# Performance work log

Hardware: AMD Instinct MI355X
Metric: run time of the kernel (lower is better)

## Reference

```python
import math
import jax, jax.numpy as jnp
import numpy as np

B, T, C = 8, 1024, 512
H = 8
NUM_FRAMES = 128  # num_tokens
NUM_ANIMALS = 8   # num_id; NUM_FRAMES * NUM_ANIMALS == T


def _linear_params(key, fan_in, fan_out):
    kw, kb = jax.random.split(key)
    bound = 1.0 / math.sqrt(fan_in)
    W = jax.random.uniform(kw, (fan_out, fan_in), jnp.float32, -bound, bound)
    b = jax.random.uniform(kb, (fan_out,), jnp.float32, -bound, bound)
    return W, b


def setup_inputs() -> dict:
    key = jax.random.key(0)
    ks = jax.random.split(key, 6)
    x = jax.random.normal(ks[0], (B, T, C), jnp.float32)
    mask = jnp.ones((B, T), jnp.float32)
    Wq, bq = _linear_params(ks[1], C, C)
    Wk, bk = _linear_params(ks[2], C, C)
    Wv, bv = _linear_params(ks[3], C, C)
    Wp, bp = _linear_params(ks[4], C, C)
    return {"x": x, "mask": mask, "Wq": Wq, "bq": bq, "Wk": Wk, "bk": bk,
            "Wv": Wv, "bv": bv, "Wp": Wp, "bp": bp}


def _block_causal_mask():
    # tril over frames, expanded so all animals within a frame attend to all
    # animals of frames <= current frame: kron(tril(F,F), ones(I,I)) -> (T,T)
    tril = jnp.tril(jnp.ones((NUM_FRAMES, NUM_FRAMES), jnp.float32))
    return jnp.kron(tril, jnp.ones((NUM_ANIMALS, NUM_ANIMALS), jnp.float32))


def reference(x, mask, Wq, bq, Wk, bk, Wv, bv, Wp, bp):
    Bx, Tx, Cx = x.shape
    d = Cx // H
    q = (x @ Wq.T + bq).reshape(Bx, Tx, H, d).transpose(0, 2, 1, 3)  # b h t d
    k = (x @ Wk.T + bk).reshape(Bx, Tx, H, d).transpose(0, 2, 1, 3)
    v = (x @ Wv.T + bv).reshape(Bx, Tx, H, d).transpose(0, 2, 1, 3)
    att = jnp.einsum('bhqd,bhkd->bhqk', q, k) * (1.0 / math.sqrt(d))
    m = _block_causal_mask()[None, None] * mask[:, None, None, :]  # (B,1,T,T)
    att = jnp.where(m == 0, -jnp.inf, att)
    att = jax.nn.softmax(att, axis=-1)
    # dropout is identity (pdrop=0.0 / eval mode)
    y = jnp.einsum('bhqk,bhkd->bhqd', att, v)
    y = y.transpose(0, 2, 1, 3).reshape(Bx, Tx, Cx)
    return y @ Wp.T + bp
```

## Files before the change

kernel.cpp:

```cpp
#include <hip/hip_runtime.h>
#include <cstdint>
#include <cstddef>

#define BB 8
#define TT 1024
#define CC 512
#define HH 8
#define DD 64
#define MM (BB*TT)

typedef short s16x4 __attribute__((ext_vector_type(4)));
typedef _Float16 f16x8 __attribute__((ext_vector_type(8)));
typedef float f32x4  __attribute__((ext_vector_type(4)));
typedef unsigned u32x4 __attribute__((ext_vector_type(4)));

__device__ __forceinline__ short f2hs(float f) {
  _Float16 h = (_Float16)f;
  return __builtin_bit_cast(short, h);
}

__device__ __forceinline__ f32x4 mfma16h(f16x8 a, f16x8 b, f32x4 c) {
  return __builtin_amdgcn_mfma_f32_16x16x32_f16(a, b, c, 0, 0, 0);
}

__device__ __forceinline__ void gload_lds16(const void* g, void* l) {
  __builtin_amdgcn_global_load_lds(
      (const __attribute__((address_space(1))) unsigned int*)g,
      (__attribute__((address_space(3))) unsigned int*)l, 16, 0, 0);
}

__global__ void prep_kernel(const float* __restrict__ x,
                            const float* __restrict__ mask,
                            const float* __restrict__ Wq,
                            const float* __restrict__ Wk,
                            const float* __restrict__ Wv,
                            const float* __restrict__ Wp,
                            short* __restrict__ Xh,
                            short* __restrict__ Wqkv,
                            short* __restrict__ Wpc,
                            float* __restrict__ maskAdd) {
  const int NXv = MM * CC / 4;
  const int NWv = CC * CC / 4;
  const int NM = BB * TT;
  int stride = gridDim.x * blockDim.x;
  for (int i = blockIdx.x * blockDim.x + threadIdx.x; i < NXv + 4 * NWv + NM; i += stride) {
    if (i < NXv) {
      int e = i * 4;
      float4 v = *(const float4*)(x + e);
      s16x4 h = {f2hs(v.x), f2hs(v.y), f2hs(v.z), f2hs(v.w)};
      *(s16x4*)(Xh + e) = h;
    } else if (i < NXv + 4 * NWv) {
      int wi = i - NXv;
      int wsel = wi >> 16;
      int idx = wi & 65535;
      int r = idx >> 7, c = (idx & 127) << 2;
      const float* W = (wsel == 0) ? Wq : (wsel == 1) ? Wk : (wsel == 2) ? Wv : Wp;
      float4 v = *(const float4*)(W + (size_t)r * CC + c);
      s16x4 h = {f2hs(v.x), f2hs(v.y), f2hs(v.z), f2hs(v.w)};
      short* dst = (wsel < 3) ? (Wqkv + (size_t)(wsel * 512 + r) * CC + c)
                              : (Wpc + (size_t)r * CC + c);
      *(s16x4*)dst = h;
    } else {
      int mi = i - NXv - 4 * NWv;
      maskAdd[mi] = (mask[mi] == 0.f) ? -1e30f : 0.f;
    }
  }
}

template <int BN, int EPI>
__global__ __launch_bounds__(512, 4) void gemm_kernel(
    const short* __restrict__ A, const short* __restrict__ Bw,
    const float* __restrict__ b0, const float* __restrict__ b1,
    const float* __restrict__ b2,
    short* __restrict__ qo, short* __restrict__ ko, short* __restrict__ vt,
    float* __restrict__ outp) {
  constexpr int MR = 4;
  constexpr int NR = BN / 64;
  constexpr int ABYT = 128 * 128;
  constexpr int TILE = ABYT + BN * 128;
  constexpr int NT = 8;
  constexpr int BL = BN / 64;
  __shared__ __align__(1024) char smem[2 * TILE];

  const int tid = threadIdx.x;
  const int lane = tid & 63;
  const int w = tid >> 6;
  const int wm = w >> 2, wn = w & 3;
  const int l15 = lane & 15, lg = lane >> 4;
  const int lsw = (l15 & 7) << 4;
  const int sr8 = lane >> 3;
  const int scbsw = ((lane & 7) * 16) ^ (sr8 << 4);

  const int rowA = blockIdx.x * 128;
  const int rowB = blockIdx.y * BN;
  const char* Ab = (const char*)A + (size_t)(rowA + sr8) * 1024 + scbsw;
  const char* Bb = (const char*)Bw + (size_t)(rowB + sr8) * 1024 + scbsw;

  f32x4 acc[MR][NR] = {};

  auto STAGE_A = [&](char* dst, int kt) {
#pragma unroll
    for (int g = 0; g < 2; ++g) {
      int r0 = (w * 2 + g) * 8;
      gload_lds16(Ab + (size_t)r0 * 1024 + (size_t)kt * 128, dst + r0 * 128);
    }
  };
  auto STAGE_B = [&](char* dst, int kt) {
#pragma unroll
    for (int g = 0; g < BL; ++g) {
      int r0 = (w * BL + g) * 8;
      gload_lds16(Bb + (size_t)r0 * 1024 + (size_t)kt * 128, dst + ABYT + r0 * 128);
    }
  };
  auto RDA2 = [&](const char* buf, int mh, int kk, f16x8* af) {
#pragma unroll
    for (int i = 0; i < 2; ++i) {
      int row = wm * 64 + (mh * 2 + i) * 16 + l15;
      af[i] = *(const f16x8*)(buf + row * 128 + ((kk * 64 + lg * 16) ^ lsw));
    }
  };
  auto RDBk = [&](const char* buf, int kk, f16x8* bfr) {
#pragma unroll
    for (int j = 0; j < NR; ++j) {
      int row = wn * (BN / 4) + j * 16 + l15;
      bfr[j] = *(const f16x8*)(buf + ABYT + row * 128 + ((kk * 64 + lg * 16) ^ lsw));
    }
  };

  STAGE_A(smem, 0);
  STAGE_B(smem, 0);
  asm volatile("s_waitcnt vmcnt(0)" ::: "memory");
  __builtin_amdgcn_s_barrier();

  for (int t = 0; t < NT; ++t) {
    char* bufp = smem + (t & 1) * TILE;
    char* bufn = smem + ((t + 1) & 1) * TILE;
    f16x8 af[2], bfr[NR];

#define PH(MH)                                                                \
  __builtin_amdgcn_s_barrier();                                               \
  asm volatile("s_waitcnt lgkmcnt(0)" ::: "memory");                          \
  __builtin_amdgcn_sched_barrier(0);                                          \
  __builtin_amdgcn_s_setprio(1);                                              \
  _Pragma("unroll")                                                           \
  for (int i = 0; i < 2; ++i)                                                 \
    _Pragma("unroll")                                                         \
    for (int j = 0; j < NR; ++j)                                              \
      acc[(MH) * 2 + i][j] = mfma16h(af[i], bfr[j], acc[(MH) * 2 + i][j]);    \
  __builtin_amdgcn_s_setprio(0);

    RDBk(bufp, 0, bfr);
    RDA2(bufp, 0, 0, af);
    if (t + 1 < NT) STAGE_A(bufn, t + 1);
    PH(0)
    RDA2(bufp, 1, 0, af);
    if (t + 1 < NT) STAGE_B(bufn, t + 1);
    PH(1)
    RDBk(bufp, 1, bfr);
    RDA2(bufp, 1, 1, af);
    PH(1)
    RDA2(bufp, 0, 1, af);
    PH(0)
#undef PH
    asm volatile("s_waitcnt vmcnt(0)" ::: "memory");
    __builtin_amdgcn_s_barrier();
  }

#pragma unroll
  for (int m = 0; m < MR; ++m) {
    int rbase = rowA + wm * 64 + m * 16 + lg * 4;
#pragma unroll
    for (int n = 0; n < NR; ++n) {
      int col = rowB + wn * (BN / 4) + n * 16 + l15;
#pragma unroll
      for (int j = 0; j < 4; ++j) {
        float v = acc[m][n][j];
        int r = rbase + j;
        if constexpr (EPI == 0) {
          int b = r >> 10, t = r & 1023;
          int wsel = col >> 9, c = col & 511;
          int h = c >> 6, dd = c & 63;
          int bh = b * HH + h;
          if (wsel == 0) {
            qo[((size_t)bh * TT + t) * DD + dd] = f2hs((v + b0[c]) * 0.125f);
          } else if (wsel == 1) {
            ko[((size_t)bh * TT + t) * DD + dd] = f2hs(v + b1[c]);
          } else {
            vt[((size_t)bh * DD + dd) * TT + t] = f2hs(v + b2[c]);
          }
        } else {
          outp[(size_t)r * CC + col] = v + b0[col];
        }
      }
    }
  }
}

__global__ __launch_bounds__(256, 4) void attn_kernel(
    const short* __restrict__ q, const short* __restrict__ k,
    const short* __restrict__ vt, const float* __restrict__ maskAdd,
    short* __restrict__ Yh) {
  const int blk = blockIdx.x;
  const int k4 = blk >> 8;
  const int r = blk & 255;
  const int bh = r >> 2;
  const int j4 = r & 3;
  const int qb = (k4 & 1) ? ((k4 & 2) ? (4 + j4) : j4)
                          : ((k4 & 2) ? (11 - j4) : (15 - j4));
  const int b = bh >> 3, h = bh & 7;
  const int tid = threadIdx.x;
  const int lane = tid & 63;
  const int w = tid >> 6;
  const int l15 = lane & 15, lg = lane >> 4;
  const int lsw = (l15 & 7) << 4;

  __shared__ short Ks[2][64 * 64];
  __shared__ short Vs[2][64 * 64];

  const short* kbh = k + (size_t)bh * TT * DD;
  const short* vbh = vt + (size_t)bh * DD * TT;

  const int sr32 = tid >> 3;
  const int scb = (tid & 7) * 16;

  auto STAGE = [&](int bs, int tile) {
#pragma unroll
    for (int g = 0; g < 2; ++g) {
      int row = g * 32 + sr32;
      int sw = (row & 7) << 4;
      gload_lds16((const char*)kbh + ((size_t)tile * 64 + row) * 128 + (scb ^ sw),
                  (char*)&Ks[bs][0] + row * 128);
      gload_lds16((const char*)vbh + (size_t)row * 2048 + tile * 128 + (scb ^ sw),
                  (char*)&Vs[bs][0] + row * 128);
    }
  };

  const int qrow = qb * 64 + w * 16 + l15;
  const short* qptr = q + ((size_t)bh * TT + qrow) * DD;
  f16x8 qf0 = *(const f16x8*)(qptr + lg * 8);
  f16x8 qf1 = *(const f16x8*)(qptr + 32 + lg * 8);

  f32x4 yacc[4] = {};
  float mrun = -1e30f, lpart = 0.f;

  const int srcA = (((2 * lg) & 3) << 4) + l15;
  const int srcB = (((2 * lg + 1) & 3) << 4) + l15;
  const bool hiSel = (lg >= 2);

  STAGE(0, 0);
  __syncthreads();

  int buf = 0;
  for (int jt = 0; jt <= qb; ++jt) {
    if (jt < qb) STAGE(buf ^ 1, jt + 1);

    f32x4 sacc[4];
#pragma unroll
    for (int n = 0; n < 4; ++n)
      sacc[n] = *(const f32x4*)(maskAdd + (size_t)b * TT + jt * 64 + n * 16 + lg * 4);
    __builtin_amdgcn_s_setprio(1);
#pragma unroll
    for (int c = 0; c < 2; ++c) {
      f16x8 qc = (c == 0) ? qf0 : qf1;
#pragma unroll
      for (int n = 0; n < 4; ++n) {
        int krow = n * 16 + l15;
        const f16x8 kf = *(const f16x8*)((const char*)&Ks[buf][0] + krow * 128 + ((c * 64 + lg * 16) ^ lsw));
        sacc[n] = mfma16h(kf, qc, sacc[n]);
      }
    }
    __builtin_amdgcn_s_setprio(0);
    if (jt == qb) {
      const int qloc8 = (w * 16 + l15) >> 3;
#pragma unroll
      for (int n = 0; n < 4; ++n)
#pragma unroll
        for (int jj = 0; jj < 4; ++jj) {
          int kloc = n * 16 + lg * 4 + jj;
          if ((kloc >> 3) > qloc8) sacc[n][jj] = -1e30f;
        }
    }
    float t0 = fmaxf(fmaxf(sacc[0][0], sacc[0][1]), fmaxf(sacc[0][2], sacc[0][3]));
    float t1 = fmaxf(fmaxf(sacc[1][0], sacc[1][1]), fmaxf(sacc[1][2], sacc[1][3]));
    float t2 = fmaxf(fmaxf(sacc[2][0], sacc[2][1]), fmaxf(sacc[2][2], sacc[2][3]));
    float t3 = fmaxf(fmaxf(sacc[3][0], sacc[3][1]), fmaxf(sacc[3][2], sacc[3][3]));
    float pmL = fmaxf(fmaxf(t0, t1), fmaxf(t2, t3));
    if (!__all(pmL <= mrun + 8.0f)) {
      float pm = fmaxf(pmL, __shfl_xor(pmL, 16));
      pm = fmaxf(pm, __shfl_xor(pm, 32));
      float mnew = fmaxf(mrun, pm);
      float alpha = __expf(mrun - mnew);
      mrun = mnew;
      lpart *= alpha;
      float ab[4];
#pragma unroll
      for (int jj = 0; jj < 4; ++jj) ab[jj] = __shfl(alpha, lg * 4 + jj);
#pragma unroll
      for (int dt = 0; dt < 4; ++dt)
#pragma unroll
        for (int jj = 0; jj < 4; ++jj) yacc[dt][jj] *= ab[jj];
    }
    unsigned pk2[4][2];
    float lps = 0.f;
#pragma unroll
    for (int n = 0; n < 4; ++n) {
      float p0 = __expf(sacc[n][0] - mrun);
      float p1 = __expf(sacc[n][1] - mrun);
      float p2 = __expf(sacc[n][2] - mrun);
      float p3 = __expf(sacc[n][3] - mrun);
      lps += (p0 + p1) + (p2 + p3);
      pk2[n][0] = __builtin_bit_cast(unsigned, __builtin_amdgcn_cvt_pkrtz(p0, p1));
      pk2[n][1] = __builtin_bit_cast(unsigned, __builtin_amdgcn_cvt_pkrtz(p2, p3));
    }
    lpart += lps;
    f16x8 pa[2];
#pragma unroll
    for (int c = 0; c < 2; ++c) {
      unsigned a0 = __shfl(pk2[2 * c][0], srcA);
      unsigned a1 = __shfl(pk2[2 * c][1], srcA);
      unsigned a2 = __shfl(pk2[2 * c][0], srcB);
      unsigned a3 = __shfl(pk2[2 * c][1], srcB);
      unsigned b0 = __shfl(pk2[2 * c + 1][0], srcA);
      unsigned b1 = __shfl(pk2[2 * c + 1][1], srcA);
      unsigned b2 = __shfl(pk2[2 * c + 1][0], srcB);
      unsigned b3 = __shfl(pk2[2 * c + 1][1], srcB);
      u32x4 tv = {hiSel ? b0 : a0, hiSel ? b1 : a1, hiSel ? b2 : a2, hiSel ? b3 : a3};
      pa[c] = __builtin_bit_cast(f16x8, tv);
    }
    __builtin_amdgcn_s_setprio(1);
#pragma unroll
    for (int c = 0; c < 2; ++c) {
#pragma unroll
      for (int dt = 0; dt < 4; ++dt) {
        int vrow = dt * 16 + l15;
        const f16x8 vf = *(const f16x8*)((const char*)&Vs[buf][0] + vrow * 128 + ((c * 64 + lg * 16) ^ lsw));
        yacc[dt] = mfma16h(pa[c], vf, yacc[dt]);
      }
    }
    __builtin_amdgcn_s_setprio(0);

    __syncthreads();
    buf ^= 1;
  }

  float lr = lpart;
  lr += __shfl_xor(lr, 16);
  lr += __shfl_xor(lr, 32);
  float lb[4];
#pragma unroll
  for (int jj = 0; jj < 4; ++jj) lb[jj] = 1.f / __shfl(lr, lg * 4 + jj);
#pragma unroll
  for (int dt = 0; dt < 4; ++dt) {
    int col = h * DD + dt * 16 + l15;
#pragma unroll
    for (int jj = 0; jj < 4; ++jj) {
      int row = b * TT + qb * 64 + w * 16 + lg * 4 + jj;
      float y = yacc[dt][jj] * lb[jj];
      Yh[(size_t)row * CC + col] = f2hs(y);
    }
  }
}

extern "C" void kernel_launch(void* const* d_in, const int* in_sizes, int n_in,
                              void* d_out, int out_size, void* d_ws, size_t ws_size,
                              hipStream_t stream) {
  const float* x    = (const float*)d_in[0];
  const float* mask = (const float*)d_in[1];
  const float* Wq   = (const float*)d_in[2];
  const float* bq   = (const float*)d_in[3];
  const float* Wk   = (const float*)d_in[4];
  const float* bk   = (const float*)d_in[5];
  const float* Wv   = (const float*)d_in[6];
  const float* bv   = (const float*)d_in[7];
  const float* Wp   = (const float*)d_in[8];
  const float* bp   = (const float*)d_in[9];
  float* out = (float*)d_out;

  char* ws = (char*)d_ws;
  short* Xh   = (short*)(ws);
  short* Wqkv = (short*)(ws + (size_t)8 * 1048576);
  short* Wpc  = (short*)(ws + (size_t)10 * 1048576);
  short* qo   = (short*)(ws + (size_t)11 * 1048576);
  short* ko   = (short*)(ws + (size_t)19 * 1048576);
  short* vt   = (short*)(ws + (size_t)27 * 1048576);
  short* Yh   = (short*)(ws + (size_t)35 * 1048576);
  float* maskAdd = (float*)(ws + (size_t)43 * 1048576);

  prep_kernel<<<2048, 256, 0, stream>>>(x, mask, Wq, Wk, Wv, Wp, Xh, Wqkv, Wpc, maskAdd);

  gemm_kernel<192, 0><<<dim3(64, 8), 512, 0, stream>>>(
      Xh, Wqkv, bq, bk, bv, qo, ko, vt, nullptr);

  attn_kernel<<<dim3(1024), 256, 0, stream>>>(qo, ko, vt, maskAdd, Yh);

  gemm_kernel<128, 1><<<dim3(64, 4), 512, 0, stream>>>(
      Yh, Wpc, bp, nullptr, nullptr, nullptr, nullptr, nullptr, out);
}
```

Before: 73.33 us.

## Rewrite GEMMs to stage only A in LDS and load B fragments directly from global

Replaces the 512-thread GEMM with a 256-thread variant that double-buffers only the A tile in shared memory, while each wave reads its B (weight) fragments straight from global memory into registers. Tile shapes change to 128x96 for the QKV projection and 64x64 for the output projection, which gives more, smaller blocks. The aim is less LDS traffic and footprint and more occupancy, plus dropping the finely interleaved barrier schedule. In exchange, weight fragments are re-read from global/L2 by each wave with a latency that is not hidden, and the per-phase scheduling hints are lost.

```diff
diff --git a/kernel.cpp b/kernel.cpp
--- a/kernel.cpp
+++ b/kernel.cpp
@@ -67,111 +67,87 @@
   }
 }
 
-template <int BN, int EPI>
-__global__ __launch_bounds__(512, 4) void gemm_kernel(
+template <int BM, int BN, int EPI>
+__global__ __launch_bounds__(256, 4) void gemm2_kernel(
     const short* __restrict__ A, const short* __restrict__ Bw,
     const float* __restrict__ b0, const float* __restrict__ b1,
     const float* __restrict__ b2,
     short* __restrict__ qo, short* __restrict__ ko, short* __restrict__ vt,
     float* __restrict__ outp) {
-  constexpr int MR = 4;
-  constexpr int NR = BN / 64;
-  constexpr int ABYT = 128 * 128;
-  constexpr int TILE = ABYT + BN * 128;
+  constexpr int MR = BM / 32;
+  constexpr int NR = BN / 32;
+  constexpr int ABYT = BM * 128;
   constexpr int NT = 8;
-  constexpr int BL = BN / 64;
-  __shared__ __align__(1024) char smem[2 * TILE];
+  __shared__ __align__(1024) char smem[2 * ABYT];
 
   const int tid = threadIdx.x;
   const int lane = tid & 63;
   const int w = tid >> 6;
-  const int wm = w >> 2, wn = w & 3;
+  const int wm = w >> 1, wn = w & 1;
   const int l15 = lane & 15, lg = lane >> 4;
   const int lsw = (l15 & 7) << 4;
-  const int sr8 = lane >> 3;
-  const int scbsw = ((lane & 7) * 16) ^ (sr8 << 4);
-
-  const int rowA = blockIdx.x * 128;
+
+  const int rowA = blockIdx.x * BM;
   const int rowB = blockIdx.y * BN;
-  const char* Ab = (const char*)A + (size_t)(rowA + sr8) * 1024 + scbsw;
-  const char* Bb = (const char*)Bw + (size_t)(rowB + sr8) * 1024 + scbsw;
+
+  const int srow = tid >> 3;
+  const int scbsw = ((tid & 7) * 16) ^ ((srow & 7) << 4);
+  const char* Ab = (const char*)A + (size_t)(rowA + srow) * 1024 + scbsw;
+
+  auto STAGE_A = [&](char* dst, int kt) {
+#pragma unroll
+    for (int g = 0; g < BM / 32; ++g) {
+      gload_lds16(Ab + (size_t)g * 32 * 1024 + (size_t)kt * 128,
+                  dst + (g * 32 + srow) * 128);
+    }
+  };
+
+  const char* bB = (const char*)Bw +
+                   (size_t)(rowB + wn * (BN / 2) + l15) * 1024 + lg * 16;
 
   f32x4 acc[MR][NR] = {};
 
-  auto STAGE_A = [&](char* dst, int kt) {
-#pragma unroll
-    for (int g = 0; g < 2; ++g) {
-      int r0 = (w * 2 + g) * 8;
-      gload_lds16(Ab + (size_t)r0 * 1024 + (size_t)kt * 128, dst + r0 * 128);
-    }
-  };
-  auto STAGE_B = [&](char* dst, int kt) {
-#pragma unroll
-    for (int g = 0; g < BL; ++g) {
-      int r0 = (w * BL + g) * 8;
-      gload_lds16(Bb + (size_t)r0 * 1024 + (size_t)kt * 128, dst + ABYT + r0 * 128);
-    }
-  };
-  auto RDA2 = [&](const char* buf, int mh, int kk, f16x8* af) {
-#pragma unroll
-    for (int i = 0; i < 2; ++i) {
-      int row = wm * 64 + (mh * 2 + i) * 16 + l15;
-      af[i] = *(const f16x8*)(buf + row * 128 + ((kk * 64 + lg * 16) ^ lsw));
-    }
-  };
-  auto RDBk = [&](const char* buf, int kk, f16x8* bfr) {
-#pragma unroll
-    for (int j = 0; j < NR; ++j) {
-      int row = wn * (BN / 4) + j * 16 + l15;
-      bfr[j] = *(const f16x8*)(buf + ABYT + row * 128 + ((kk * 64 + lg * 16) ^ lsw));
-    }
-  };
-
   STAGE_A(smem, 0);
-  STAGE_B(smem, 0);
-  asm volatile("s_waitcnt vmcnt(0)" ::: "memory");
-  __builtin_amdgcn_s_barrier();
+  __syncthreads();
 
   for (int t = 0; t < NT; ++t) {
-    char* bufp = smem + (t & 1) * TILE;
-    char* bufn = smem + ((t + 1) & 1) * TILE;
-    f16x8 af[2], bfr[NR];
-
-#define PH(MH)                                                                \
-  __builtin_amdgcn_s_barrier();                                               \
-  asm volatile("s_waitcnt lgkmcnt(0)" ::: "memory");                          \
-  __builtin_amdgcn_sched_barrier(0);                                          \
-  __builtin_amdgcn_s_setprio(1);                                              \
-  _Pragma("unroll")                                                           \
-  for (int i = 0; i < 2; ++i)                                                 \
-    _Pragma("unroll")                                                         \
-    for (int j = 0; j < NR; ++j)                                              \
-      acc[(MH) * 2 + i][j] = mfma16h(af[i], bfr[j], acc[(MH) * 2 + i][j]);    \
-  __builtin_amdgcn_s_setprio(0);
-
-    RDBk(bufp, 0, bfr);
-    RDA2(bufp, 0, 0, af);
+    const char* bufp = smem + (t & 1) * ABYT;
+    char* bufn = smem + ((t + 1) & 1) * ABYT;
+
+    f16x8 bfr[2][NR];
+#pragma unroll
+    for (int kk = 0; kk < 2; ++kk)
+#pragma unroll
+      for (int j = 0; j < NR; ++j)
+        bfr[kk][j] = *(const f16x8*)(bB + (size_t)j * 16 * 1024 +
+                                     (size_t)t * 128 + kk * 64);
     if (t + 1 < NT) STAGE_A(bufn, t + 1);
-    PH(0)
-    RDA2(bufp, 1, 0, af);
-    if (t + 1 < NT) STAGE_B(bufn, t + 1);
-    PH(1)
-    RDBk(bufp, 1, bfr);
-    RDA2(bufp, 1, 1, af);
-    PH(1)
-    RDA2(bufp, 0, 1, af);
-    PH(0)
-#undef PH
-    asm volatile("s_waitcnt vmcnt(0)" ::: "memory");
-    __builtin_amdgcn_s_barrier();
+
+#pragma unroll
+    for (int kk = 0; kk < 2; ++kk) {
+      f16x8 af[MR];
+#pragma unroll
+      for (int m = 0; m < MR; ++m) {
+        int row = wm * (BM / 2) + m * 16 + l15;
+        af[m] = *(const f16x8*)(bufp + row * 128 + ((kk * 64 + lg * 16) ^ lsw));
+      }
+      __builtin_amdgcn_s_setprio(1);
+#pragma unroll
+      for (int m = 0; m < MR; ++m)
+#pragma unroll
+        for (int j = 0; j < NR; ++j)
+          acc[m][j] = mfma16h(af[m], bfr[kk][j], acc[m][j]);
+      __builtin_amdgcn_s_setprio(0);
+    }
+    __syncthreads();
   }
 
 #pragma unroll
   for (int m = 0; m < MR; ++m) {
-    int rbase = rowA + wm * 64 + m * 16 + lg * 4;
+    int rbase = rowA + wm * (BM / 2) + m * 16 + lg * 4;
 #pragma unroll
     for (int n = 0; n < NR; ++n) {
-      int col = rowB + wn * (BN / 4) + n * 16 + l15;
+      int col = rowB + wn * (BN / 2) + n * 16 + l15;
 #pragma unroll
       for (int j = 0; j < 4; ++j) {
         float v = acc[m][n][j];
@@ -388,11 +364,11 @@
 
   prep_kernel<<<2048, 256, 0, stream>>>(x, mask, Wq, Wk, Wv, Wp, Xh, Wqkv, Wpc, maskAdd);
 
-  gemm_kernel<192, 0><<<dim3(64, 8), 512, 0, stream>>>(
+  gemm2_kernel<128, 96, 0><<<dim3(64, 16), 256, 0, stream>>>(
       Xh, Wqkv, bq, bk, bv, qo, ko, vt, nullptr);
 
   attn_kernel<<<dim3(1024), 256, 0, stream>>>(qo, ko, vt, maskAdd, Yh);
 
-  gemm_kernel<128, 1><<<dim3(64, 4), 512, 0, stream>>>(
+  gemm2_kernel<64, 64, 1><<<dim3(128, 8), 256, 0, stream>>>(
       Yh, Wpc, bp, nullptr, nullptr, nullptr, nullptr, nullptr, out);
 }
```

Measured after the change: 103.6 us. +41.3%, slower.

## Fuse fp32-to-fp16 conversion of x into the QKV GEMM A-tile load

Applied to the files above, without the earlier changes.

The prep kernel no longer converts the whole activation tensor x to fp16 in a separate pass. A new QKV GEMM kernel loads fp32 x into registers, converts it with packed conversions and writes the swizzled fp16 tile into LDS, while weights are still staged with direct global-to-LDS loads. This removes a full write and re-read of an 8 MB intermediate. In exchange the A-tile load now goes through registers and each of the eight column blocks reads twice as many bytes of x.

```diff
diff --git a/kernel.cpp b/kernel.cpp
--- a/kernel.cpp
+++ b/kernel.cpp
@@ -18,6 +18,9 @@
   _Float16 h = (_Float16)f;
   return __builtin_bit_cast(short, h);
 }
+__device__ __forceinline__ unsigned pkh(float a, float b) {
+  return __builtin_bit_cast(unsigned, __builtin_amdgcn_cvt_pkrtz(a, b));
+}
 
 __device__ __forceinline__ f32x4 mfma16h(f16x8 a, f16x8 b, f32x4 c) {
   return __builtin_amdgcn_mfma_f32_16x16x32_f16(a, b, c, 0, 0, 0);
@@ -29,30 +32,21 @@
       (__attribute__((address_space(3))) unsigned int*)l, 16, 0, 0);
 }
 
-__global__ void prep_kernel(const float* __restrict__ x,
-                            const float* __restrict__ mask,
+__global__ void prep_kernel(const float* __restrict__ mask,
                             const float* __restrict__ Wq,
                             const float* __restrict__ Wk,
                             const float* __restrict__ Wv,
                             const float* __restrict__ Wp,
-                            short* __restrict__ Xh,
                             short* __restrict__ Wqkv,
                             short* __restrict__ Wpc,
                             float* __restrict__ maskAdd) {
-  const int NXv = MM * CC / 4;
   const int NWv = CC * CC / 4;
   const int NM = BB * TT;
   int stride = gridDim.x * blockDim.x;
-  for (int i = blockIdx.x * blockDim.x + threadIdx.x; i < NXv + 4 * NWv + NM; i += stride) {
-    if (i < NXv) {
-      int e = i * 4;
-      float4 v = *(const float4*)(x + e);
-      s16x4 h = {f2hs(v.x), f2hs(v.y), f2hs(v.z), f2hs(v.w)};
-      *(s16x4*)(Xh + e) = h;
-    } else if (i < NXv + 4 * NWv) {
-      int wi = i - NXv;
-      int wsel = wi >> 16;
-      int idx = wi & 65535;
+  for (int i = blockIdx.x * blockDim.x + threadIdx.x; i < 4 * NWv + NM; i += stride) {
+    if (i < 4 * NWv) {
+      int wsel = i >> 16;
+      int idx = i & 65535;
       int r = idx >> 7, c = (idx & 127) << 2;
       const float* W = (wsel == 0) ? Wq : (wsel == 1) ? Wk : (wsel == 2) ? Wv : Wp;
       float4 v = *(const float4*)(W + (size_t)r * CC + c);
@@ -61,8 +55,148 @@
                               : (Wpc + (size_t)r * CC + c);
       *(s16x4*)dst = h;
     } else {
-      int mi = i - NXv - 4 * NWv;
+      int mi = i - 4 * NWv;
       maskAdd[mi] = (mask[mi] == 0.f) ? -1e30f : 0.f;
+    }
+  }
+}
+
+__global__ __launch_bounds__(512, 4) void gemm_qkv_kernel(
+    const float* __restrict__ X, const short* __restrict__ Bw,
+    const float* __restrict__ b0, const float* __restrict__ b1,
+    const float* __restrict__ b2,
+    short* __restrict__ qo, short* __restrict__ ko, short* __restrict__ vt) {
+  constexpr int BN = 192;
+  constexpr int MR = 4;
+  constexpr int NR = BN / 64;
+  constexpr int ABYT = 128 * 128;
+  constexpr int TILE = ABYT + BN * 128;
+  constexpr int NT = 8;
+  constexpr int BL = BN / 64;
+  __shared__ __align__(1024) char smem[2 * TILE];
+
+  const int tid = threadIdx.x;
+  const int lane = tid & 63;
+  const int w = tid >> 6;
+  const int wm = w >> 2, wn = w & 3;
+  const int l15 = lane & 15, lg = lane >> 4;
+  const int lsw = (l15 & 7) << 4;
+  const int sr8 = lane >> 3;
+  const int scbsw = ((lane & 7) * 16) ^ (sr8 << 4);
+
+  const int rowA = blockIdx.x * 128;
+  const int rowB = blockIdx.y * BN;
+  const char* Bb = (const char*)Bw + (size_t)(rowB + sr8) * 1024 + scbsw;
+
+  const int arow = tid >> 2;
+  const int achk = tid & 3;
+  const char* Xb = (const char*)X + (size_t)(rowA + arow) * 2048 + achk * 64;
+  const int asw = (arow & 7) << 4;
+  float4 xr[4];
+
+  auto LOADX = [&](int kt) {
+#pragma unroll
+    for (int i = 0; i < 4; ++i)
+      xr[i] = *(const float4*)(Xb + (size_t)kt * 256 + i * 16);
+  };
+  auto CVTW = [&](char* dst) {
+    u32x4 lo = {pkh(xr[0].x, xr[0].y), pkh(xr[0].z, xr[0].w),
+                pkh(xr[1].x, xr[1].y), pkh(xr[1].z, xr[1].w)};
+    u32x4 hi = {pkh(xr[2].x, xr[2].y), pkh(xr[2].z, xr[2].w),
+                pkh(xr[3].x, xr[3].y), pkh(xr[3].z, xr[3].w)};
+    char* base = dst + arow * 128;
+    *(u32x4*)(base + ((achk * 32) ^ asw)) = lo;
+    *(u32x4*)(base + ((achk * 32 + 16) ^ asw)) = hi;
+  };
+  auto STAGE_B = [&](char* dst, int kt) {
+#pragma unroll
+    for (int g = 0; g < BL; ++g) {
+      int r0 = (w * BL + g) * 8;
+      gload_lds16(Bb + (size_t)r0 * 1024 + (size_t)kt * 128, dst + ABYT + r0 * 128);
+    }
+  };
+  auto RDA2 = [&](const char* buf, int mh, int kk, f16x8* af) {
+#pragma unroll
+    for (int i = 0; i < 2; ++i) {
+      int row = wm * 64 + (mh * 2 + i) * 16 + l15;
+      af[i] = *(const f16x8*)(buf + row * 128 + ((kk * 64 + lg * 16) ^ lsw));
+    }
+  };
+  auto RDBk = [&](const char* buf, int kk, f16x8* bfr) {
+#pragma unroll
+    for (int j = 0; j < NR; ++j) {
+      int row = wn * (BN / 4) + j * 16 + l15;
+      bfr[j] = *(const f16x8*)(buf + ABYT + row * 128 + ((kk * 64 + lg * 16) ^ lsw));
+    }
+  };
+
+  f32x4 acc[MR][NR] = {};
+
+  LOADX(0);
+  STAGE_B(smem, 0);
+  asm volatile("s_waitcnt vmcnt(0)" ::: "memory");
+  CVTW(smem);
+  asm volatile("s_waitcnt lgkmcnt(0)" ::: "memory");
+  __builtin_amdgcn_s_barrier();
+
+  for (int t = 0; t < NT; ++t) {
+    char* bufp = smem + (t & 1) * TILE;
+    char* bufn = smem + ((t + 1) & 1) * TILE;
+    f16x8 af[2], bfr[NR];
+
+#define PH(MH)                                                                \
+  __builtin_amdgcn_s_barrier();                                               \
+  asm volatile("s_waitcnt lgkmcnt(0)" ::: "memory");                          \
+  __builtin_amdgcn_sched_barrier(0);                                          \
+  __builtin_amdgcn_s_setprio(1);                                              \
+  _Pragma("unroll")                                                           \
+  for (int i = 0; i < 2; ++i)                                                 \
+    _Pragma("unroll")                                                         \
+    for (int j = 0; j < NR; ++j)                                              \
+      acc[(MH) * 2 + i][j] = mfma16h(af[i], bfr[j], acc[(MH) * 2 + i][j]);    \
+  __builtin_amdgcn_s_setprio(0);
+
+    RDBk(bufp, 0, bfr);
+    RDA2(bufp, 0, 0, af);
+    if (t + 1 < NT) LOADX(t + 1);
+    PH(0)
+    RDA2(bufp, 1, 0, af);
+    if (t + 1 < NT) STAGE_B(bufn, t + 1);
+    PH(1)
+    RDBk(bufp, 1, bfr);
+    RDA2(bufp, 1, 1, af);
+    PH(1)
+    RDA2(bufp, 0, 1, af);
+    PH(0)
+#undef PH
+    asm volatile("s_waitcnt vmcnt(0)" ::: "memory");
+    if (t + 1 < NT) CVTW(bufn);
+    asm volatile("s_waitcnt lgkmcnt(0)" ::: "memory");
+    __builtin_amdgcn_s_barrier();
+  }
+
+#pragma unroll
+  for (int m = 0; m < MR; ++m) {
+    int rbase = rowA + wm * 64 + m * 16 + lg * 4;
+#pragma unroll
+    for (int n = 0; n < NR; ++n) {
+      int col = rowB + wn * (BN / 4) + n * 16 + l15;
+#pragma unroll
+      for (int j = 0; j < 4; ++j) {
+        float v = acc[m][n][j];
+        int r = rbase + j;
+        int b = r >> 10, t = r & 1023;
+        int wsel = col >> 9, c = col & 511;
+        int h = c >> 6, dd = c & 63;
+        int bh = b * HH + h;
+        if (wsel == 0) {
+          qo[((size_t)bh * TT + t) * DD + dd] = f2hs((v + b0[c]) * 0.125f);
+        } else if (wsel == 1) {
+          ko[((size_t)bh * TT + t) * DD + dd] = f2hs(v + b1[c]);
+        } else {
+          vt[((size_t)bh * DD + dd) * TT + t] = f2hs(v + b2[c]);
+        }
+      }
     }
   }
 }
@@ -309,8 +443,8 @@
       float p2 = __expf(sacc[n][2] - mrun);
       float p3 = __expf(sacc[n][3] - mrun);
       lps += (p0 + p1) + (p2 + p3);
-      pk2[n][0] = __builtin_bit_cast(unsigned, __builtin_amdgcn_cvt_pkrtz(p0, p1));
-      pk2[n][1] = __builtin_bit_cast(unsigned, __builtin_amdgcn_cvt_pkrtz(p2, p3));
+      pk2[n][0] = pkh(p0, p1);
+      pk2[n][1] = pkh(p2, p3);
     }
     lpart += lps;
     f16x8 pa[2];
@@ -377,7 +511,6 @@
   float* out = (float*)d_out;
 
   char* ws = (char*)d_ws;
-  short* Xh   = (short*)(ws);
   short* Wqkv = (short*)(ws + (size_t)8 * 1048576);
   short* Wpc  = (short*)(ws + (size_t)10 * 1048576);
   short* qo   = (short*)(ws + (size_t)11 * 1048576);
@@ -386,10 +519,10 @@
   short* Yh   = (short*)(ws + (size_t)35 * 1048576);
   float* maskAdd = (float*)(ws + (size_t)43 * 1048576);
 
-  prep_kernel<<<2048, 256, 0, stream>>>(x, mask, Wq, Wk, Wv, Wp, Xh, Wqkv, Wpc, maskAdd);
-
-  gemm_kernel<192, 0><<<dim3(64, 8), 512, 0, stream>>>(
-      Xh, Wqkv, bq, bk, bv, qo, ko, vt, nullptr);
+  prep_kernel<<<1024, 256, 0, stream>>>(mask, Wq, Wk, Wv, Wp, Wqkv, Wpc, maskAdd);
+
+  gemm_qkv_kernel<<<dim3(64, 8), 512, 0, stream>>>(
+      x, Wqkv, bq, bk, bv, qo, ko, vt);
 
   attn_kernel<<<dim3(1024), 256, 0, stream>>>(qo, ko, vt, maskAdd, Yh);
 
```

Result: slower. 76.68 us (+4.6%).
